# Performance work log

Measured on AMD Instinct MI355X. Metric: run time of the kernel, lower is better.

## Reference

```python
import jax, jax.numpy as jnp
import numpy as np

D = 2048; Nl = 2; Nh = 32; Nkv = 8; V = 32000; Dh = 5632; Lm = 4096
B = 1; L = 2048; E = 1e-5
DHEAD = D // Nh  # 64


def setup_inputs() -> dict:
    key = jax.random.key(0)
    ks = jax.random.split(key, 10)
    s = 0.02
    rn = lambda k, shape: jax.random.normal(k, shape, jnp.float32) * s
    emb = rn(ks[0], (V, D))
    wq = rn(ks[1], (Nl, D, D))
    wk = rn(ks[2], (Nl, D, D * Nkv // Nh))
    wv = rn(ks[3], (Nl, D, D * Nkv // Nh))
    wa = rn(ks[4], (Nl, D, D))
    wg = rn(ks[5], (Nl, D, Dh))
    wu = rn(ks[6], (Nl, D, Dh))
    wd = rn(ks[7], (Nl, Dh, D))
    w_an = jnp.ones((Nl, D), jnp.float32)
    w_fn = jnp.ones((Nl, D), jnp.float32)
    w_on = jnp.ones((D,), jnp.float32)
    w_out = rn(ks[8], (D, V))
    # RoPE tables (interleaved-pair convention, matching reshape(..., -1, 2))
    theta = 1.0 / (10000.0 ** (jnp.arange(0, DHEAD, 2, dtype=jnp.float32) / DHEAD))
    freqs = jnp.outer(jnp.arange(Lm, dtype=jnp.float32), theta)  # [Lm, DHEAD//2]
    cos = jnp.cos(freqs)
    sin = jnp.sin(freqs)
    ti = jax.random.randint(ks[9], (B, L), 0, V)
    return dict(ti=ti, emb=emb, wq=wq, wk=wk, wv=wv, wa=wa, w_an=w_an, w_fn=w_fn,
                wg=wg, wu=wu, wd=wd, w_on=w_on, w_out=w_out, cos=cos, sin=sin)


def _rmsnorm(x, w):
    return x * jax.lax.rsqrt(jnp.mean(x * x, -1, keepdims=True) + E) * w


def _rope(x, cos, sin):
    # x: [B, L, H, DHEAD]; cos/sin: [1, L, 1, DHEAD//2]; interleaved pairs
    xs = x.reshape(*x.shape[:-1], DHEAD // 2, 2)
    xr, xi = xs[..., 0], xs[..., 1]
    r1 = xr * cos - xi * sin
    i1 = xr * sin + xi * cos
    return jnp.stack([r1, i1], axis=-1).reshape(x.shape)


def reference(ti, emb, wq, wk, wv, wa, w_an, w_fn, wg, wu, wd, w_on, w_out, cos, sin):
    cos_l = cos[:L].reshape(1, L, 1, DHEAD // 2)
    sin_l = sin[:L].reshape(1, L, 1, DHEAD // 2)
    mask = jnp.triu(jnp.full((1, 1, L, L), -jnp.inf, jnp.float32), 1)
    scale = 1.0 / jnp.sqrt(jnp.float32(DHEAD))
    rep = Nh // Nkv
    x = emb[ti]  # [B, L, D]
    for l in range(Nl):
        h = _rmsnorm(x, w_an[l])
        q = (h @ wq[l]).reshape(B, L, Nh, DHEAD)
        k = (h @ wk[l]).reshape(B, L, Nkv, DHEAD)
        v = (h @ wv[l]).reshape(B, L, Nkv, DHEAD)
        q = _rope(q, cos_l, sin_l)
        k = _rope(k, cos_l, sin_l)
        kx = jnp.repeat(k, rep, axis=2)  # GQA expand -> [B, L, Nh, DHEAD]
        vx = jnp.repeat(v, rep, axis=2)
        a = jnp.einsum('blhd,bmhd->bhlm', q, kx) * scale
        p = jax.nn.softmax(a + mask, axis=-1)
        sa = jnp.einsum('bhlm,bmhd->blhd', p, vx).reshape(B, L, D)
        x = x + sa @ wa[l]
        hf = _rmsnorm(x, w_fn[l])
        x = x + (jax.nn.silu(hf @ wg[l]) * (hf @ wu[l])) @ wd[l]
    return _rmsnorm(x, w_on) @ w_out  # [B, L, V]
```

## Files before the change

kernel.cpp:

```cpp
#include <hip/hip_runtime.h>
#include <hip/hip_bf16.h>

#define DMODEL 2048
#define LSEQ   2048
#define NHEAD  32
#define NKVH   8
#define DHEAD  64
#define DFF    5632
#define VOCAB  32000

typedef __attribute__((ext_vector_type(8))) short bf16x8;
typedef __attribute__((ext_vector_type(4))) float f32x4;
typedef __attribute__((ext_vector_type(8))) unsigned short ushort8;

__device__ __forceinline__ void gload_lds16(const __hip_bfloat16* g, __hip_bfloat16* l) {
  __builtin_amdgcn_global_load_lds((const void __attribute__((address_space(1)))*)g,
                                   (void __attribute__((address_space(3)))*)l, 16, 0, 0);
}

__device__ __forceinline__ float bfbits2f(unsigned short u) {
  return __uint_as_float(((unsigned int)u) << 16);
}
__device__ __forceinline__ unsigned short f2bfbits(float f) {
  unsigned int x = __float_as_uint(f);
  return (unsigned short)((x + 0x7fffu + ((x >> 16) & 1u)) >> 16);
}

__global__ __launch_bounds__(256) void embed_k(const int* __restrict__ ti,
                                               const float* __restrict__ emb,
                                               float* __restrict__ x) {
  const int row = blockIdx.x;
  const int t = threadIdx.x;
  const int tok = ti[row];
  const float4* s = (const float4*)(emb + (size_t)tok * DMODEL);
  float4* d = (float4*)(x + (size_t)row * DMODEL);
  d[t] = s[t];
  d[t + 256] = s[t + 256];
}

__global__ __launch_bounds__(256) void rmsnorm_k(const float* __restrict__ x,
                                                 const float* __restrict__ w,
                                                 __hip_bfloat16* __restrict__ out) {
  const int row = blockIdx.x;
  const int t = threadIdx.x;
  const float4* xr = (const float4*)(x + (size_t)row * DMODEL);
  float4 a = xr[t];
  float4 b = xr[t + 256];
  float ss = a.x*a.x + a.y*a.y + a.z*a.z + a.w*a.w
           + b.x*b.x + b.y*b.y + b.z*b.z + b.w*b.w;
  #pragma unroll
  for (int m = 32; m >= 1; m >>= 1) ss += __shfl_xor(ss, m);
  __shared__ float red[4];
  if ((t & 63) == 0) red[t >> 6] = ss;
  __syncthreads();
  const float tot = red[0] + red[1] + red[2] + red[3];
  const float sc = rsqrtf(tot * (1.0f / DMODEL) + 1e-5f);
  const float4* w4 = (const float4*)w;
  float4 wa_ = w4[t], wb_ = w4[t + 256];
  __hip_bfloat16* o = out + (size_t)row * DMODEL;
  o[4*t + 0] = __float2bfloat16(a.x * sc * wa_.x);
  o[4*t + 1] = __float2bfloat16(a.y * sc * wa_.y);
  o[4*t + 2] = __float2bfloat16(a.z * sc * wa_.z);
  o[4*t + 3] = __float2bfloat16(a.w * sc * wa_.w);
  o[1024 + 4*t + 0] = __float2bfloat16(b.x * sc * wb_.x);
  o[1024 + 4*t + 1] = __float2bfloat16(b.y * sc * wb_.y);
  o[1024 + 4*t + 2] = __float2bfloat16(b.z * sc * wb_.z);
  o[1024 + 4*t + 3] = __float2bfloat16(b.w * sc * wb_.w);
}

__global__ __launch_bounds__(256) void transpose_k(const float* __restrict__ src,
                                                   __hip_bfloat16* __restrict__ dst,
                                                   int K, int N) {
  __shared__ float tile[64 * 65];
  const int kb = blockIdx.x * 64;
  const int nb = blockIdx.y * 64;
  const int t = threadIdx.x;
  #pragma unroll
  for (int i = 0; i < 16; ++i) {
    const int idx = t + 256 * i;
    const int r = idx >> 6, c = idx & 63;
    tile[r * 65 + c] = src[(size_t)(kb + r) * N + nb + c];
  }
  __syncthreads();
  #pragma unroll
  for (int i = 0; i < 16; ++i) {
    const int idx = t + 256 * i;
    const int n = idx >> 6, k = idx & 63;
    dst[(size_t)(nb + n) * K + kb + k] = __float2bfloat16(tile[k * 65 + n]);
  }
}

template <int EPI>
__global__ __launch_bounds__(256) void gemm_bt(const __hip_bfloat16* __restrict__ A,
                                               const __hip_bfloat16* __restrict__ Bt,
                                               float* __restrict__ Cf,
                                               __hip_bfloat16* __restrict__ Cb,
                                               int M, int N, int K) {
  __shared__ __align__(16) __hip_bfloat16 As[128 * 32];
  __shared__ __align__(16) __hip_bfloat16 Bs[128 * 32];
  const int tid = threadIdx.x;
  const int wave = tid >> 6;
  const int lane = tid & 63;
  const int nbx = M >> 7;
  const int nwg = nbx * (N >> 7);
  const int orig = blockIdx.y * nbx + blockIdx.x;
  const int wid = (orig & 7) * (nwg >> 3) + (orig >> 3);
  const int tm = (wid % nbx) << 7;
  const int tn = (wid / nbx) << 7;
  const int wr = (wave >> 1) * 64;
  const int wc = (wave & 1) * 64;
  const int fr = lane & 15;
  const int fg = lane >> 4;
  const f32x4 fzero = {0.f, 0.f, 0.f, 0.f};
  f32x4 acc[4][4];
  #pragma unroll
  for (int i = 0; i < 4; ++i)
    #pragma unroll
    for (int j = 0; j < 4; ++j) acc[i][j] = fzero;
  const int srow = wave * 32 + (lane >> 2);
  const int scol = (lane & 3) * 8;
  const __hip_bfloat16* gA = A + (size_t)(tm + srow) * K + scol;
  const __hip_bfloat16* gB = Bt + (size_t)(tn + srow) * K + scol;
  __hip_bfloat16* lA = &As[wave * 1024];
  __hip_bfloat16* lB = &Bs[wave * 1024];
  for (int k0 = 0; k0 < K; k0 += 32) {
    gload_lds16(gA, lA);
    gload_lds16(gA + (size_t)16 * K, lA + 512);
    gload_lds16(gB, lB);
    gload_lds16(gB + (size_t)16 * K, lB + 512);
    gA += 32; gB += 32;
    __syncthreads();
    bf16x8 af[4], bfr[4];
    #pragma unroll
    for (int i = 0; i < 4; ++i) af[i] = *(const bf16x8*)&As[(wr + i * 16 + fr) * 32 + fg * 8];
    #pragma unroll
    for (int j = 0; j < 4; ++j) bfr[j] = *(const bf16x8*)&Bs[(wc + j * 16 + fr) * 32 + fg * 8];
    #pragma unroll
    for (int i = 0; i < 4; ++i)
      #pragma unroll
      for (int j = 0; j < 4; ++j)
        acc[i][j] = __builtin_amdgcn_mfma_f32_16x16x32_bf16(af[i], bfr[j], acc[i][j], 0, 0, 0);
    __syncthreads();
  }
  #pragma unroll
  for (int i = 0; i < 4; ++i)
    #pragma unroll
    for (int j = 0; j < 4; ++j)
      #pragma unroll
      for (int r = 0; r < 4; ++r) {
        const int row = tm + wr + i * 16 + fg * 4 + r;
        const int col = tn + wc + j * 16 + fr;
        const float v = acc[i][j][r];
        if (EPI == 0) Cf[(size_t)row * N + col] = v;
        else if (EPI == 1) Cb[(size_t)row * N + col] = __float2bfloat16(v);
        else Cf[(size_t)row * N + col] += v;
      }
}

template <int EPI>
__global__ __launch_bounds__(512, 2) void gemm8p(const __hip_bfloat16* __restrict__ A,
                                                 const __hip_bfloat16* __restrict__ Bt,
                                                 float* __restrict__ Cf,
                                                 __hip_bfloat16* __restrict__ Cb,
                                                 int M, int N, int K) {
  __shared__ __align__(16) __hip_bfloat16 lds[2][2][256 * 64];
  const int tid = threadIdx.x;
  const int wave = tid >> 6;
  const int lane = tid & 63;
  const int nbx = M >> 8;
  const int nwg = nbx * (N >> 8);
  const int orig = blockIdx.y * nbx + blockIdx.x;
  const int wid = (orig & 7) * (nwg >> 3) + (orig >> 3);
  const int tm = (wid % nbx) << 8;
  const int tn = (wid / nbx) << 8;
  const int wm = wave >> 2;
  const int wn = wave & 3;
  const int fr = lane & 15;
  const int fg = lane >> 4;
  const int l3 = lane >> 3;
  const int l7 = lane & 7;
  const int swzcol = (l3 ^ l7) << 3;
  const size_t sK = (size_t)K;

  const __hip_bfloat16* pA = A + (size_t)(tm + wave * 8 + l3) * sK + swzcol;
  const __hip_bfloat16* pB = Bt + (size_t)(tn + wave * 8 + l3) * sK + swzcol;

  #pragma unroll
  for (int j = 0; j < 4; ++j) {
    gload_lds16(pA + (size_t)(j * 64) * sK, &lds[0][0][(j * 64 + wave * 8) * 64]);
    gload_lds16(pB + (size_t)(j * 64) * sK, &lds[0][1][(j * 64 + wave * 8) * 64]);
  }
  pA += 64; pB += 64;
  #pragma unroll
  for (int j = 0; j < 4; ++j) {
    gload_lds16(pA + (size_t)(j * 64) * sK, &lds[1][0][(j * 64 + wave * 8) * 64]);
    gload_lds16(pB + (size_t)(j * 64) * sK, &lds[1][1][(j * 64 + wave * 8) * 64]);
  }
  pA += 64; pB += 64;

  const f32x4 fzero = {0.f, 0.f, 0.f, 0.f};
  f32x4 acc[8][4];
  #pragma unroll
  for (int i = 0; i < 8; ++i)
    #pragma unroll
    for (int j = 0; j < 4; ++j) acc[i][j] = fzero;

  const int wmo = wm * 128;
  const int wno = wn * 64;
  const int rswz = (fr & 7) << 4;
  const int ct0 = ((fg * 16) ^ rswz) >> 1;
  const int ct1 = ((64 + fg * 16) ^ rswz) >> 1;

  asm volatile("s_waitcnt vmcnt(8)" ::: "memory");
  __builtin_amdgcn_s_barrier();
  __builtin_amdgcn_sched_barrier(0);

  const int NT = K >> 6;
  for (int kt = 0; kt < NT; ++kt) {
    const int cur = kt & 1;
    const __hip_bfloat16* LA = &lds[cur][0][0];
    const __hip_bfloat16* LB = &lds[cur][1][0];
    bf16x8 a0[4][2], a1[4][2], b0[2][2], b1[2][2];
    #pragma unroll
    for (int mi = 0; mi < 4; ++mi) {
      a0[mi][0] = *(const bf16x8*)&LA[(wmo + mi * 16 + fr) * 64 + ct0];
      a0[mi][1] = *(const bf16x8*)&LA[(wmo + mi * 16 + fr) * 64 + ct1];
    }
    #pragma unroll
    for (int ni = 0; ni < 2; ++ni) {
      b0[ni][0] = *(const bf16x8*)&LB[(wno + ni * 16 + fr) * 64 + ct0];
      b0[ni][1] = *(const bf16x8*)&LB[(wno + ni * 16 + fr) * 64 + ct1];
    }
    #pragma unroll
    for (int mi = 0; mi < 4; ++mi) {
      a1[mi][0] = *(const bf16x8*)&LA[(wmo + (4 + mi) * 16 + fr) * 64 + ct0];
      a1[mi][1] = *(const bf16x8*)&LA[(wmo + (4 + mi) * 16 + fr) * 64 + ct1];
    }
    __builtin_amdgcn_s_setprio(1);
    #pragma unroll
    for (int mi = 0; mi < 4; ++mi)
      #pragma unroll
      for (int ni = 0; ni < 2; ++ni) {
        acc[mi][ni] = __builtin_amdgcn_mfma_f32_16x16x32_bf16(a0[mi][0], b0[ni][0], acc[mi][ni], 0, 0, 0);
        acc[mi][ni] = __builtin_amdgcn_mfma_f32_16x16x32_bf16(a0[mi][1], b0[ni][1], acc[mi][ni], 0, 0, 0);
      }
    __builtin_amdgcn_s_setprio(0);
    #pragma unroll
    for (int ni = 0; ni < 2; ++ni) {
      b1[ni][0] = *(const bf16x8*)&LB[(wno + (2 + ni) * 16 + fr) * 64 + ct0];
      b1[ni][1] = *(const bf16x8*)&LB[(wno + (2 + ni) * 16 + fr) * 64 + ct1];
    }
    __builtin_amdgcn_s_setprio(1);
    #pragma unroll
    for (int mi = 0; mi < 4; ++mi)
      #pragma unroll
      for (int ni = 0; ni < 2; ++ni) {
        acc[4 + mi][ni] = __builtin_amdgcn_mfma_f32_16x16x32_bf16(a1[mi][0], b0[ni][0], acc[4 + mi][ni], 0, 0, 0);
        acc[4 + mi][ni] = __builtin_amdgcn_mfma_f32_16x16x32_bf16(a1[mi][1], b0[ni][1], acc[4 + mi][ni], 0, 0, 0);
      }
    #pragma unroll
    for (int mi = 0; mi < 4; ++mi)
      #pragma unroll
      for (int ni = 0; ni < 2; ++ni) {
        acc[4 + mi][2 + ni] = __builtin_amdgcn_mfma_f32_16x16x32_bf16(a1[mi][0], b1[ni][0], acc[4 + mi][2 + ni], 0, 0, 0);
        acc[4 + mi][2 + ni] = __builtin_amdgcn_mfma_f32_16x16x32_bf16(a1[mi][1], b1[ni][1], acc[4 + mi][2 + ni], 0, 0, 0);
      }
    #pragma unroll
    for (int mi = 0; mi < 4; ++mi)
      #pragma unroll
      for (int ni = 0; ni < 2; ++ni) {
        acc[mi][2 + ni] = __builtin_amdgcn_mfma_f32_16x16x32_bf16(a0[mi][0], b1[ni][0], acc[mi][2 + ni], 0, 0, 0);
        acc[mi][2 + ni] = __builtin_amdgcn_mfma_f32_16x16x32_bf16(a0[mi][1], b1[ni][1], acc[mi][2 + ni], 0, 0, 0);
      }
    __builtin_amdgcn_s_setprio(0);
    __builtin_amdgcn_s_barrier();
    __builtin_amdgcn_sched_barrier(0);
    const bool pre = (kt + 2 < NT);
    if (pre) {
      #pragma unroll
      for (int q = 0; q < 4; ++q) {
        gload_lds16(pA + (size_t)(q * 64) * sK, &lds[cur][0][(q * 64 + wave * 8) * 64]);
        gload_lds16(pB + (size_t)(q * 64) * sK, &lds[cur][1][(q * 64 + wave * 8) * 64]);
      }
      pA += 64; pB += 64;
    }
    if (kt + 1 < NT) {
      if (pre) asm volatile("s_waitcnt vmcnt(8)" ::: "memory");
      else     asm volatile("s_waitcnt vmcnt(0)" ::: "memory");
      __builtin_amdgcn_s_barrier();
      __builtin_amdgcn_sched_barrier(0);
    }
  }
  #pragma unroll
  for (int mf = 0; mf < 8; ++mf)
    #pragma unroll
    for (int nf = 0; nf < 4; ++nf)
      #pragma unroll
      for (int r = 0; r < 4; ++r) {
        const int row = tm + wmo + mf * 16 + fg * 4 + r;
        const int col = tn + wno + nf * 16 + fr;
        const float v = acc[mf][nf][r];
        if (EPI == 0) Cf[(size_t)row * N + col] = v;
        else if (EPI == 1) Cb[(size_t)row * N + col] = __float2bfloat16(v);
        else Cf[(size_t)row * N + col] += v;
      }
}

__global__ __launch_bounds__(256) void rope_k(__hip_bfloat16* __restrict__ qkv,
                                              const float* __restrict__ cosT,
                                              const float* __restrict__ sinT) {
  const int row = blockIdx.x;
  const int t = threadIdx.x;
  unsigned int* base = (unsigned int*)(qkv + (size_t)row * 3072);
  #pragma unroll
  for (int p = t; p < 1280; p += 256) {
    const int hp = p >> 5;
    const int i = p & 31;
    const unsigned int packed = base[hp * 32 + i];
    const float x0 = bfbits2f((unsigned short)(packed & 0xffffu));
    const float x1 = bfbits2f((unsigned short)(packed >> 16));
    const float c = cosT[row * 32 + i];
    const float s = sinT[row * 32 + i];
    const float r0 = x0 * c - x1 * s;
    const float r1 = x0 * s + x1 * c;
    base[hp * 32 + i] = (unsigned int)f2bfbits(r0) | ((unsigned int)f2bfbits(r1) << 16);
  }
}

__global__ __launch_bounds__(256) void attn_k(const __hip_bfloat16* __restrict__ qkv,
                                              __hip_bfloat16* __restrict__ out) {
  const int h = blockIdx.x;
  const int qt = blockIdx.y;
  const int tid = threadIdx.x;
  const int wave = tid >> 6;
  const int lane = tid & 63;
  const int fr = lane & 15;
  const int fg = lane >> 4;
  const int qb = qt * 64;
  const int kcol = DMODEL + (h >> 2) * DHEAD;
  const int vcol = DMODEL + NKVH * DHEAD + (h >> 2) * DHEAD;
  __shared__ __align__(16) __hip_bfloat16 Ks[64 * 72];
  __shared__ __align__(16) __hip_bfloat16 Vt[64 * 72];
  __shared__ __align__(16) __hip_bfloat16 Ps[4][16 * 72];
  bf16x8 qf[2];
  {
    const __hip_bfloat16* qp = qkv + (size_t)(qb + wave * 16 + fr) * 3072 + h * DHEAD + fg * 8;
    qf[0] = *(const bf16x8*)qp;
    qf[1] = *(const bf16x8*)(qp + 32);
  }
  const f32x4 fzero = {0.f, 0.f, 0.f, 0.f};
  float m_run[4], l_run[4];
  f32x4 o[4];
  #pragma unroll
  for (int r = 0; r < 4; ++r) { m_run[r] = -1e30f; l_run[r] = 0.f; }
  #pragma unroll
  for (int c = 0; c < 4; ++c) o[c] = fzero;

  const int sr = tid >> 2;
  const int sc = (tid & 3) * 16;
  for (int t = 0; t <= qt; ++t) {
    const __hip_bfloat16* kp = qkv + (size_t)(t * 64 + sr) * 3072 + kcol + sc;
    *(float4*)&Ks[sr * 72 + sc] = *(const float4*)kp;
    *(float4*)&Ks[sr * 72 + sc + 8] = *(const float4*)(kp + 8);
    const __hip_bfloat16* vp = qkv + (size_t)(t * 64 + sr) * 3072 + vcol + sc;
    ushort8 v0 = *(const ushort8*)vp;
    ushort8 v1 = *(const ushort8*)(vp + 8);
    unsigned short* vt = (unsigned short*)Vt;
    #pragma unroll
    for (int i = 0; i < 8; ++i) {
      vt[(sc + i) * 72 + sr] = v0[i];
      vt[(sc + 8 + i) * 72 + sr] = v1[i];
    }
    __syncthreads();
    f32x4 s[4];
    #pragma unroll
    for (int c = 0; c < 4; ++c) {
      s[c] = fzero;
      #pragma unroll
      for (int ks = 0; ks < 2; ++ks) {
        bf16x8 kf = *(const bf16x8*)&Ks[(c * 16 + fr) * 72 + ks * 32 + fg * 8];
        s[c] = __builtin_amdgcn_mfma_f32_16x16x32_bf16(qf[ks], kf, s[c], 0, 0, 0);
      }
    }
    const int rowg = qb + wave * 16 + fg * 4;
    #pragma unroll
    for (int c = 0; c < 4; ++c)
      #pragma unroll
      for (int r = 0; r < 4; ++r) {
        float v = s[c][r] * 0.125f;
        if (t * 64 + c * 16 + fr > rowg + r) v = -1e30f;
        s[c][r] = v;
      }
    #pragma unroll
    for (int r = 0; r < 4; ++r) {
      float pm = fmaxf(fmaxf(s[0][r], s[1][r]), fmaxf(s[2][r], s[3][r]));
      pm = fmaxf(pm, __shfl_xor(pm, 1));
      pm = fmaxf(pm, __shfl_xor(pm, 2));
      pm = fmaxf(pm, __shfl_xor(pm, 4));
      pm = fmaxf(pm, __shfl_xor(pm, 8));
      const float mn = fmaxf(m_run[r], pm);
      const float al = __expf(m_run[r] - mn);
      m_run[r] = mn;
      float rs = 0.f;
      #pragma unroll
      for (int c = 0; c < 4; ++c) { float p = __expf(s[c][r] - mn); s[c][r] = p; rs += p; }
      rs += __shfl_xor(rs, 1);
      rs += __shfl_xor(rs, 2);
      rs += __shfl_xor(rs, 4);
      rs += __shfl_xor(rs, 8);
      l_run[r] = l_run[r] * al + rs;
      #pragma unroll
      for (int c = 0; c < 4; ++c) o[c][r] *= al;
    }
    unsigned short* pw = (unsigned short*)Ps[wave];
    #pragma unroll
    for (int c = 0; c < 4; ++c)
      #pragma unroll
      for (int r = 0; r < 4; ++r)
        pw[(fg * 4 + r) * 72 + c * 16 + fr] = f2bfbits(s[c][r]);
    #pragma unroll
    for (int ks = 0; ks < 2; ++ks) {
      bf16x8 pf = *(const bf16x8*)&Ps[wave][fr * 72 + ks * 32 + fg * 8];
      #pragma unroll
      for (int c = 0; c < 4; ++c) {
        bf16x8 vf = *(const bf16x8*)&Vt[(c * 16 + fr) * 72 + ks * 32 + fg * 8];
        o[c] = __builtin_amdgcn_mfma_f32_16x16x32_bf16(pf, vf, o[c], 0, 0, 0);
      }
    }
    __syncthreads();
  }
  #pragma unroll
  for (int c = 0; c < 4; ++c)
    #pragma unroll
    for (int r = 0; r < 4; ++r)
      out[(size_t)(qb + wave * 16 + fg * 4 + r) * DMODEL + h * DHEAD + c * 16 + fr] =
          __float2bfloat16(o[c][r] / l_run[r]);
}

__global__ __launch_bounds__(256) void silu_k(const __hip_bfloat16* __restrict__ gu,
                                              __hip_bfloat16* __restrict__ mb) {
  const int row = blockIdx.x;
  const int t = threadIdx.x;
  const ushort8* g8 = (const ushort8*)(gu + (size_t)row * (2 * DFF));
  const ushort8* u8 = (const ushort8*)(gu + (size_t)row * (2 * DFF) + DFF);
  ushort8* m8 = (ushort8*)(mb + (size_t)row * DFF);
  for (int j = t; j * 8 < DFF; j += 256) {
    ushort8 g = g8[j], u = u8[j];
    ushort8 ov;
    #pragma unroll
    for (int i = 0; i < 8; ++i) {
      const float gf = bfbits2f(g[i]);
      const float uf = bfbits2f(u[i]);
      ov[i] = f2bfbits(gf / (1.f + __expf(-gf)) * uf);
    }
    m8[j] = ov;
  }
}

extern "C" void kernel_launch(void* const* d_in, const int* in_sizes, int n_in,
                              void* d_out, int out_size, void* d_ws, size_t ws_size,
                              hipStream_t stream) {
  const int* ti = (const int*)d_in[0];
  const float* emb = (const float*)d_in[1];
  const float* wq = (const float*)d_in[2];
  const float* wk = (const float*)d_in[3];
  const float* wv = (const float*)d_in[4];
  const float* wa = (const float*)d_in[5];
  const float* w_an = (const float*)d_in[6];
  const float* w_fn = (const float*)d_in[7];
  const float* wg = (const float*)d_in[8];
  const float* wu = (const float*)d_in[9];
  const float* wd = (const float*)d_in[10];
  const float* w_on = (const float*)d_in[11];
  const float* w_out = (const float*)d_in[12];
  const float* cosT = (const float*)d_in[13];
  const float* sinT = (const float*)d_in[14];
  float* outp = (float*)d_out;

  char* ws = (char*)d_ws;
  float* x            = (float*)(ws + 0);
  __hip_bfloat16* h   = (__hip_bfloat16*)(ws + 16777216);
  __hip_bfloat16* qkv = (__hip_bfloat16*)(ws + 25165824);
  __hip_bfloat16* att = (__hip_bfloat16*)(ws + 37748736);
  __hip_bfloat16* gu  = (__hip_bfloat16*)(ws + 46137344);
  __hip_bfloat16* mb  = (__hip_bfloat16*)(ws + 92274688);
  __hip_bfloat16* wTqkv = (__hip_bfloat16*)(ws + 115343360);
  __hip_bfloat16* wTa   = (__hip_bfloat16*)(ws + 127926272);
  __hip_bfloat16* wTgu  = (__hip_bfloat16*)(ws + 136314880);
  __hip_bfloat16* wTd   = (__hip_bfloat16*)(ws + 182452224);
  __hip_bfloat16* wTout = (__hip_bfloat16*)(ws + 25165824);
  (void)in_sizes; (void)n_in; (void)out_size; (void)ws_size;

  const dim3 blk(256);
  embed_k<<<2048, blk, 0, stream>>>(ti, emb, x);
  for (int l = 0; l < 2; ++l) {
    transpose_k<<<dim3(32, 32), blk, 0, stream>>>(wq + (size_t)l * 2048 * 2048, wTqkv, 2048, 2048);
    transpose_k<<<dim3(32, 8),  blk, 0, stream>>>(wk + (size_t)l * 2048 * 512, wTqkv + (size_t)2048 * 2048, 2048, 512);
    transpose_k<<<dim3(32, 8),  blk, 0, stream>>>(wv + (size_t)l * 2048 * 512, wTqkv + (size_t)2560 * 2048, 2048, 512);
    transpose_k<<<dim3(32, 32), blk, 0, stream>>>(wa + (size_t)l * 2048 * 2048, wTa, 2048, 2048);
    transpose_k<<<dim3(32, 88), blk, 0, stream>>>(wg + (size_t)l * 2048 * 5632, wTgu, 2048, 5632);
    transpose_k<<<dim3(32, 88), blk, 0, stream>>>(wu + (size_t)l * 2048 * 5632, wTgu + (size_t)5632 * 2048, 2048, 5632);
    transpose_k<<<dim3(88, 32), blk, 0, stream>>>(wd + (size_t)l * 5632 * 2048, wTd, 5632, 2048);

    rmsnorm_k<<<2048, blk, 0, stream>>>(x, w_an + l * 2048, h);
    gemm_bt<1><<<dim3(16, 24), blk, 0, stream>>>(h, wTqkv, nullptr, qkv, 2048, 3072, 2048);
    rope_k<<<2048, blk, 0, stream>>>(qkv, cosT, sinT);
    attn_k<<<dim3(32, 32), blk, 0, stream>>>(qkv, att);
    gemm_bt<2><<<dim3(16, 16), blk, 0, stream>>>(att, wTa, x, nullptr, 2048, 2048, 2048);

    rmsnorm_k<<<2048, blk, 0, stream>>>(x, w_fn + l * 2048, h);
    gemm8p<1><<<dim3(8, 44), dim3(512), 0, stream>>>(h, wTgu, nullptr, gu, 2048, 11264, 2048);
    silu_k<<<2048, blk, 0, stream>>>(gu, mb);
    gemm_bt<2><<<dim3(16, 16), blk, 0, stream>>>(mb, wTd, x, nullptr, 2048, 2048, 5632);
  }
  transpose_k<<<dim3(32, 500), blk, 0, stream>>>(w_out, wTout, 2048, 32000);
  rmsnorm_k<<<2048, blk, 0, stream>>>(x, w_on, h);
  gemm8p<0><<<dim3(8, 125), dim3(512), 0, stream>>>(h, wTout, outp, nullptr, 2048, 32000, 2048);
}
```

Before: 1.529 ms.

## Interleave global-to-LDS prefetch loads between MFMA phases in GEMM main loop

Splits the GEMM k-loop into four MFMA phases separated by barriers and issues the next tile's global_load_lds prefetches in pieces between phases, instead of all at once after the compute. Each A/B sub-block is reloaded only once all waves have finished reading that region of the current buffer. The goal is to spread memory traffic across the compute and keep the MFMA units busy while loads are in flight. In exchange it adds several extra workgroup barriers per iteration, and correctness depends on the region-ordering and vmcnt accounting being exactly right.

```diff
diff --git a/kernel.cpp b/kernel.cpp
--- a/kernel.cpp
+++ b/kernel.cpp
@@ -220,7 +220,11 @@
     const int cur = kt & 1;
     const __hip_bfloat16* LA = &lds[cur][0][0];
     const __hip_bfloat16* LB = &lds[cur][1][0];
+    __hip_bfloat16* SA = &lds[cur][0][0];
+    __hip_bfloat16* SB = &lds[cur][1][0];
+    const bool pre = (kt + 2 < NT);
     bf16x8 a0[4][2], a1[4][2], b0[2][2], b1[2][2];
+
     #pragma unroll
     for (int mi = 0; mi < 4; ++mi) {
       a0[mi][0] = *(const bf16x8*)&LA[(wmo + mi * 16 + fr) * 64 + ct0];
@@ -231,33 +235,59 @@
       b0[ni][0] = *(const bf16x8*)&LB[(wno + ni * 16 + fr) * 64 + ct0];
       b0[ni][1] = *(const bf16x8*)&LB[(wno + ni * 16 + fr) * 64 + ct1];
     }
+    asm volatile("s_waitcnt lgkmcnt(8)" ::: "memory");
+    __builtin_amdgcn_s_barrier();
+    asm volatile("s_waitcnt lgkmcnt(0)" ::: "memory");
+    __builtin_amdgcn_sched_barrier(0);
+    __builtin_amdgcn_s_setprio(1);
+    #pragma unroll
+    for (int mi = 0; mi < 4; ++mi)
+      #pragma unroll
+      for (int ni = 0; ni < 2; ++ni) {
+        acc[mi][ni] = __builtin_amdgcn_mfma_f32_16x16x32_bf16(a0[mi][0], b0[ni][0], acc[mi][ni], 0, 0, 0);
+        acc[mi][ni] = __builtin_amdgcn_mfma_f32_16x16x32_bf16(a0[mi][1], b0[ni][1], acc[mi][ni], 0, 0, 0);
+      }
+    __builtin_amdgcn_s_setprio(0);
+    __builtin_amdgcn_s_barrier();
+    __builtin_amdgcn_sched_barrier(0);
+
     #pragma unroll
     for (int mi = 0; mi < 4; ++mi) {
       a1[mi][0] = *(const bf16x8*)&LA[(wmo + (4 + mi) * 16 + fr) * 64 + ct0];
       a1[mi][1] = *(const bf16x8*)&LA[(wmo + (4 + mi) * 16 + fr) * 64 + ct1];
     }
+    if (pre) {
+      gload_lds16(pA, &SA[(wave * 8) * 64]);
+      gload_lds16(pA + (size_t)128 * sK, &SA[(128 + wave * 8) * 64]);
+    }
+    __builtin_amdgcn_s_barrier();
+    asm volatile("s_waitcnt lgkmcnt(0)" ::: "memory");
+    __builtin_amdgcn_sched_barrier(0);
     __builtin_amdgcn_s_setprio(1);
     #pragma unroll
     for (int mi = 0; mi < 4; ++mi)
       #pragma unroll
       for (int ni = 0; ni < 2; ++ni) {
-        acc[mi][ni] = __builtin_amdgcn_mfma_f32_16x16x32_bf16(a0[mi][0], b0[ni][0], acc[mi][ni], 0, 0, 0);
-        acc[mi][ni] = __builtin_amdgcn_mfma_f32_16x16x32_bf16(a0[mi][1], b0[ni][1], acc[mi][ni], 0, 0, 0);
+        acc[4 + mi][ni] = __builtin_amdgcn_mfma_f32_16x16x32_bf16(a1[mi][0], b0[ni][0], acc[4 + mi][ni], 0, 0, 0);
+        acc[4 + mi][ni] = __builtin_amdgcn_mfma_f32_16x16x32_bf16(a1[mi][1], b0[ni][1], acc[4 + mi][ni], 0, 0, 0);
       }
     __builtin_amdgcn_s_setprio(0);
+    __builtin_amdgcn_s_barrier();
+    __builtin_amdgcn_sched_barrier(0);
+
     #pragma unroll
     for (int ni = 0; ni < 2; ++ni) {
       b1[ni][0] = *(const bf16x8*)&LB[(wno + (2 + ni) * 16 + fr) * 64 + ct0];
       b1[ni][1] = *(const bf16x8*)&LB[(wno + (2 + ni) * 16 + fr) * 64 + ct1];
     }
+    if (pre) {
+      gload_lds16(pA + (size_t)64 * sK, &SA[(64 + wave * 8) * 64]);
+      gload_lds16(pA + (size_t)192 * sK, &SA[(192 + wave * 8) * 64]);
+    }
+    __builtin_amdgcn_s_barrier();
+    asm volatile("s_waitcnt lgkmcnt(0)" ::: "memory");
+    __builtin_amdgcn_sched_barrier(0);
     __builtin_amdgcn_s_setprio(1);
-    #pragma unroll
-    for (int mi = 0; mi < 4; ++mi)
-      #pragma unroll
-      for (int ni = 0; ni < 2; ++ni) {
-        acc[4 + mi][ni] = __builtin_amdgcn_mfma_f32_16x16x32_bf16(a1[mi][0], b0[ni][0], acc[4 + mi][ni], 0, 0, 0);
-        acc[4 + mi][ni] = __builtin_amdgcn_mfma_f32_16x16x32_bf16(a1[mi][1], b0[ni][1], acc[4 + mi][ni], 0, 0, 0);
-      }
     #pragma unroll
     for (int mi = 0; mi < 4; ++mi)
       #pragma unroll
@@ -265,6 +295,21 @@
         acc[4 + mi][2 + ni] = __builtin_amdgcn_mfma_f32_16x16x32_bf16(a1[mi][0], b1[ni][0], acc[4 + mi][2 + ni], 0, 0, 0);
         acc[4 + mi][2 + ni] = __builtin_amdgcn_mfma_f32_16x16x32_bf16(a1[mi][1], b1[ni][1], acc[4 + mi][2 + ni], 0, 0, 0);
       }
+    __builtin_amdgcn_s_setprio(0);
+    __builtin_amdgcn_s_barrier();
+    __builtin_amdgcn_sched_barrier(0);
+
+    if (pre) {
+      #pragma unroll
+      for (int j = 0; j < 4; ++j)
+        gload_lds16(pB + (size_t)(j * 64) * sK, &SB[(j * 64 + wave * 8) * 64]);
+      pA += 64; pB += 64;
+    }
+    if (pre)              asm volatile("s_waitcnt vmcnt(8)" ::: "memory");
+    else if (kt + 1 < NT) asm volatile("s_waitcnt vmcnt(0)" ::: "memory");
+    __builtin_amdgcn_s_barrier();
+    __builtin_amdgcn_sched_barrier(0);
+    __builtin_amdgcn_s_setprio(1);
     #pragma unroll
     for (int mi = 0; mi < 4; ++mi)
       #pragma unroll
@@ -275,21 +320,6 @@
     __builtin_amdgcn_s_setprio(0);
     __builtin_amdgcn_s_barrier();
     __builtin_amdgcn_sched_barrier(0);
-    const bool pre = (kt + 2 < NT);
-    if (pre) {
-      #pragma unroll
-      for (int q = 0; q < 4; ++q) {
-        gload_lds16(pA + (size_t)(q * 64) * sK, &lds[cur][0][(q * 64 + wave * 8) * 64]);
-        gload_lds16(pB + (size_t)(q * 64) * sK, &lds[cur][1][(q * 64 + wave * 8) * 64]);
-      }
-      pA += 64; pB += 64;
-    }
-    if (kt + 1 < NT) {
-      if (pre) asm volatile("s_waitcnt vmcnt(8)" ::: "memory");
-      else     asm volatile("s_waitcnt vmcnt(0)" ::: "memory");
-      __builtin_amdgcn_s_barrier();
-      __builtin_amdgcn_sched_barrier(0);
-    }
   }
   #pragma unroll
   for (int mf = 0; mf < 8; ++mf)
```

After: 1.504 ms. About the same (-1.7%).
